# Performance work log

Measured on AMD Instinct MI355X. Metric: run time of the kernel, lower is better.

## Reference

```python
import math
import jax, jax.numpy as jnp
import numpy as np

NUM_HEADS = 16


def apply_rope(x, cos, sin):
    """x: (B,H,S,D); cos,sin: (S,D). Interleaved-pair rotation, matching torch code:
    uses even-indexed entries of cos/sin for both halves of each pair."""
    x1 = x[..., ::2]          # (B,H,S,D/2)
    x2 = x[..., 1::2]
    c = cos[:, ::2]           # (S,D/2)
    s = sin[:, ::2]
    rx_even = x1 * c - x2 * s
    rx_odd = x1 * s + x2 * c
    return jnp.stack([rx_even, rx_odd], axis=-1).reshape(x.shape)


def setup_inputs() -> dict:
    key = jax.random.key(0)
    ks = jax.random.split(key, 4)
    B, S, E = 4, 1024, 1024
    H, D = NUM_HEADS, E // NUM_HEADS
    x = jax.random.normal(ks[0], (B, S, E), dtype=jnp.float32)
    # realistic RoPE tables
    inv_freq = 1.0 / (10000.0 ** (np.arange(0, D, 2, dtype=np.float32) / D))
    pos = np.arange(S, dtype=np.float32)
    ang = pos[:, None] * inv_freq[None, :]            # (S, D/2)
    ang = np.repeat(ang, 2, axis=-1)                  # (S, D)
    cos = jnp.asarray(np.cos(ang), dtype=jnp.float32)
    sin = jnp.asarray(np.sin(ang), dtype=jnp.float32)
    attn_mask = jnp.zeros((S, S), dtype=jnp.float32)
    w_qkv = jax.random.normal(ks[1], (3 * E, E), dtype=jnp.float32) * (E ** -0.5)
    w_out = jax.random.normal(ks[2], (E, E), dtype=jnp.float32) * (E ** -0.5)
    b_out = jnp.zeros((E,), dtype=jnp.float32)
    return {"x": x, "attn_mask": attn_mask, "cos": cos, "sin": sin,
            "w_qkv": w_qkv, "w_out": w_out, "b_out": b_out}


def reference(x, attn_mask, cos, sin, w_qkv, w_out, b_out):
    B, S, E = x.shape
    H = NUM_HEADS
    D = E // H
    qkv = x @ w_qkv.T                                  # (B,S,3E)
    qkv = qkv.reshape(B, S, 3, H, D).transpose(2, 0, 3, 1, 4)  # (3,B,H,S,D)
    q, k, v = qkv[0], qkv[1], qkv[2]
    q = apply_rope(q, cos, sin)
    k = apply_rope(k, cos, sin)
    scores = jnp.einsum('bhqd,bhkd->bhqk', q, k) / math.sqrt(D)
    scores = scores + attn_mask                        # broadcast (S,S)
    attn = jax.nn.softmax(scores, axis=-1)
    out = jnp.einsum('bhqk,bhkd->bhqd', attn, v)
    out = out.transpose(0, 2, 1, 3).reshape(B, S, E)   # (B,S,E)
    return out @ w_out.T + b_out, attn
```

## Files before the change

kernel.cpp:

```cpp
#include <hip/hip_runtime.h>
#include <hip/hip_bf16.h>
#include <math.h>

#define S_ 1024
#define E_ 1024
#define H_ 16
#define D_ 64

typedef __attribute__((ext_vector_type(8))) short sv8;
typedef __attribute__((ext_vector_type(4))) short sv4;
typedef __attribute__((ext_vector_type(4))) float f4;

__device__ __forceinline__ short f2b(float f) {
  union { __hip_bfloat16 h; short s; } u;
  u.h = __float2bfloat16(f);
  return u.s;
}

__global__ void k_cvt(const float* __restrict__ x, const float* __restrict__ wqkv,
                      const float* __restrict__ wout, short* __restrict__ dst) {
  const long total = 8388608 / 4;
  for (long i = (long)blockIdx.x * blockDim.x + threadIdx.x; i < total;
       i += (long)gridDim.x * blockDim.x) {
    const long e = i * 4;
    float4 v;
    if (e < 4194304L)       v = *(const float4*)&x[e];
    else if (e < 7340032L)  v = *(const float4*)&wqkv[e - 4194304L];
    else                    v = *(const float4*)&wout[e - 7340032L];
    sv4 o;
    o[0] = f2b(v.x); o[1] = f2b(v.y); o[2] = f2b(v.z); o[3] = f2b(v.w);
    *(sv4*)&dst[e] = o;
  }
}

__global__ __launch_bounds__(256) void k_qkv_rope(
    const short* __restrict__ Xb, const short* __restrict__ Wb,
    const float* __restrict__ cosb, const float* __restrict__ sinb,
    short* __restrict__ qk, short* __restrict__ vT) {
  const int t = threadIdx.x;
  const int w = t >> 6, lane = t & 63, lr = lane & 15, lh = lane >> 4;
  const int m_w = blockIdx.y * 128 + (w & 1) * 64;
  const int n_w = blockIdx.x * 128 + (w >> 1) * 64;
  f4 acc[4][4] = {};
  for (int k0 = 0; k0 < 1024; k0 += 32) {
    sv8 a[4], b[4];
#pragma unroll
    for (int mt = 0; mt < 4; ++mt)
      a[mt] = *(const sv8*)&Xb[(size_t)(m_w + mt * 16 + lr) * 1024 + k0 + lh * 8];
#pragma unroll
    for (int nt = 0; nt < 4; ++nt)
      b[nt] = *(const sv8*)&Wb[(size_t)(n_w + nt * 16 + lr) * 1024 + k0 + lh * 8];
#pragma unroll
    for (int mt = 0; mt < 4; ++mt)
#pragma unroll
      for (int nt = 0; nt < 4; ++nt)
        acc[mt][nt] = __builtin_amdgcn_mfma_f32_16x16x32_bf16(a[mt], b[nt], acc[mt][nt], 0, 0, 0);
  }
#pragma unroll
  for (int nt = 0; nt < 4; ++nt) {
    const int n = n_w + nt * 16 + lr;
    const int which = n >> 10;
    const int e = n & 1023, h = e >> 6, d = e & 63;
#pragma unroll
    for (int mt = 0; mt < 4; ++mt) {
#pragma unroll
      for (int g = 0; g < 4; ++g) {
        const int m = m_w + mt * 16 + lh * 4 + g;
        const int bb = m >> 10, s = m & 1023;
        float v = acc[mt][nt][g];
        if (which < 2) {
          const float part = __shfl_xor(v, 1);
          const float c = cosb[s * 64 + (d & ~1)];
          const float sn = sinb[s * 64 + (d & ~1)];
          v = (d & 1) ? (part * sn + v * c) : (v * c - part * sn);
          qk[(size_t)which * 4194304 + ((size_t)((bb * 16 + h) * 1024 + s)) * 64 + d] = f2b(v);
        } else {
          vT[((size_t)((bb * 16 + h) * 64 + d)) * 1024 + s] = f2b(v);
        }
      }
    }
  }
}

__global__ __launch_bounds__(256) void k_attn(
    const short* __restrict__ qk, const short* __restrict__ vT,
    const float* __restrict__ mask, float* __restrict__ attn,
    short* __restrict__ ows) {
  __shared__ float Pl[4][32][68];
  __shared__ float redm[4][32], reds[4][32];
  const int t = threadIdx.x;
  const int w = t >> 6, lane = t & 63, lr = lane & 15, lh = lane >> 4;
  const int bh = blockIdx.y, q0 = blockIdx.x * 32;
  const int b = bh >> 4, h = bh & 15;
  const short* q = qk;
  const short* kk = qk + 4194304;

  sv8 qa[2][2];
#pragma unroll
  for (int mt = 0; mt < 2; ++mt)
#pragma unroll
    for (int kt = 0; kt < 2; ++kt)
      qa[mt][kt] = *(const sv8*)&q[((size_t)bh * 1024 + q0 + mt * 16 + lr) * 64 + kt * 32 + lh * 8];

  f4 acc[2][16] = {};
#pragma unroll
  for (int ct = 0; ct < 16; ++ct) {
    sv8 kb[2];
#pragma unroll
    for (int kt = 0; kt < 2; ++kt)
      kb[kt] = *(const sv8*)&kk[((size_t)bh * 1024 + w * 256 + ct * 16 + lr) * 64 + kt * 32 + lh * 8];
#pragma unroll
    for (int mt = 0; mt < 2; ++mt)
#pragma unroll
      for (int kt = 0; kt < 2; ++kt)
        acc[mt][ct] = __builtin_amdgcn_mfma_f32_16x16x32_bf16(qa[mt][kt], kb[kt], acc[mt][ct], 0, 0, 0);
  }

#pragma unroll
  for (int mt = 0; mt < 2; ++mt)
#pragma unroll
    for (int ct = 0; ct < 16; ++ct)
#pragma unroll
      for (int g = 0; g < 4; ++g)
        acc[mt][ct][g] = acc[mt][ct][g] * 0.125f +
            mask[(size_t)(q0 + mt * 16 + lh * 4 + g) * 1024 + w * 256 + ct * 16 + lr];

#pragma unroll
  for (int mt = 0; mt < 2; ++mt)
#pragma unroll
    for (int g = 0; g < 4; ++g) {
      float m = -1e30f;
#pragma unroll
      for (int ct = 0; ct < 16; ++ct) m = fmaxf(m, acc[mt][ct][g]);
      m = fmaxf(m, __shfl_xor(m, 1));
      m = fmaxf(m, __shfl_xor(m, 2));
      m = fmaxf(m, __shfl_xor(m, 4));
      m = fmaxf(m, __shfl_xor(m, 8));
      if (lr == 0) redm[w][mt * 16 + lh * 4 + g] = m;
    }
  __syncthreads();

#pragma unroll
  for (int mt = 0; mt < 2; ++mt)
#pragma unroll
    for (int g = 0; g < 4; ++g) {
      const int row = mt * 16 + lh * 4 + g;
      const float m = fmaxf(fmaxf(redm[0][row], redm[1][row]),
                            fmaxf(redm[2][row], redm[3][row]));
      float s = 0.f;
#pragma unroll
      for (int ct = 0; ct < 16; ++ct) {
        const float e = __expf(acc[mt][ct][g] - m);
        acc[mt][ct][g] = e;
        s += e;
      }
      s += __shfl_xor(s, 1);
      s += __shfl_xor(s, 2);
      s += __shfl_xor(s, 4);
      s += __shfl_xor(s, 8);
      if (lr == 0) reds[w][row] = s;
    }
  __syncthreads();

#pragma unroll
  for (int mt = 0; mt < 2; ++mt)
#pragma unroll
    for (int g = 0; g < 4; ++g) {
      const int row = mt * 16 + lh * 4 + g;
      const float r = 1.f / (reds[0][row] + reds[1][row] + reds[2][row] + reds[3][row]);
#pragma unroll
      for (int ct = 0; ct < 16; ++ct) {
        const float p = acc[mt][ct][g] * r;
        acc[mt][ct][g] = p;
        attn[((size_t)bh * 1024 + q0 + row) * 1024 + w * 256 + ct * 16 + lr] = p;
      }
    }

  f4 of[2][4] = {};
  for (int sc = 0; sc < 4; ++sc) {
    asm volatile("s_waitcnt lgkmcnt(0)" ::: "memory");
#pragma unroll
    for (int mt = 0; mt < 2; ++mt)
#pragma unroll
      for (int ci = 0; ci < 4; ++ci)
#pragma unroll
        for (int g = 0; g < 4; ++g)
          Pl[w][mt * 16 + lh * 4 + g][ci * 16 + lr] = acc[mt][sc * 4 + ci][g];
#pragma unroll
    for (int ktl = 0; ktl < 2; ++ktl) {
      sv8 pa[2];
#pragma unroll
      for (int mt = 0; mt < 2; ++mt) {
        const float* pp = &Pl[w][mt * 16 + lr][ktl * 32 + lh * 8];
        const float4 x0 = *(const float4*)pp;
        const float4 x1 = *(const float4*)(pp + 4);
        sv8 r;
        r[0] = f2b(x0.x); r[1] = f2b(x0.y); r[2] = f2b(x0.z); r[3] = f2b(x0.w);
        r[4] = f2b(x1.x); r[5] = f2b(x1.y); r[6] = f2b(x1.z); r[7] = f2b(x1.w);
        pa[mt] = r;
      }
#pragma unroll
      for (int nt = 0; nt < 4; ++nt) {
        const sv8 vb = *(const sv8*)&vT[((size_t)bh * 64 + nt * 16 + lr) * 1024 +
                                        w * 256 + sc * 64 + ktl * 32 + lh * 8];
#pragma unroll
        for (int mt = 0; mt < 2; ++mt)
          of[mt][nt] = __builtin_amdgcn_mfma_f32_16x16x32_bf16(pa[mt], vb, of[mt][nt], 0, 0, 0);
      }
    }
  }

  asm volatile("s_waitcnt lgkmcnt(0)" ::: "memory");
#pragma unroll
  for (int mt = 0; mt < 2; ++mt)
#pragma unroll
    for (int nt = 0; nt < 4; ++nt)
#pragma unroll
      for (int g = 0; g < 4; ++g)
        Pl[w][mt * 16 + lh * 4 + g][nt * 16 + lr] = of[mt][nt][g];
  __syncthreads();
  {
    const int row = t >> 3, c8 = (t & 7) * 8;
    sv8 oa;
#pragma unroll
    for (int j = 0; j < 8; ++j) {
      const float v = Pl[0][row][c8 + j] + Pl[1][row][c8 + j] +
                      Pl[2][row][c8 + j] + Pl[3][row][c8 + j];
      oa[j] = f2b(v);
    }
    *(sv8*)&ows[((size_t)(b * 1024) + q0 + row) * 1024 + h * 64 + c8] = oa;
  }
}

__global__ __launch_bounds__(256) void k_outproj(
    const short* __restrict__ Ob, const short* __restrict__ Wb,
    const float* __restrict__ bout, float* __restrict__ out) {
  const int t = threadIdx.x;
  const int w = t >> 6, lane = t & 63, lr = lane & 15, lh = lane >> 4;
  const int m_w = blockIdx.y * 128 + (w & 1) * 64;
  const int n_w = blockIdx.x * 128 + (w >> 1) * 64;
  f4 acc[4][4] = {};
  for (int k0 = 0; k0 < 1024; k0 += 32) {
    sv8 a[4], b[4];
#pragma unroll
    for (int mt = 0; mt < 4; ++mt)
      a[mt] = *(const sv8*)&Ob[(size_t)(m_w + mt * 16 + lr) * 1024 + k0 + lh * 8];
#pragma unroll
    for (int nt = 0; nt < 4; ++nt)
      b[nt] = *(const sv8*)&Wb[(size_t)(n_w + nt * 16 + lr) * 1024 + k0 + lh * 8];
#pragma unroll
    for (int mt = 0; mt < 4; ++mt)
#pragma unroll
      for (int nt = 0; nt < 4; ++nt)
        acc[mt][nt] = __builtin_amdgcn_mfma_f32_16x16x32_bf16(a[mt], b[nt], acc[mt][nt], 0, 0, 0);
  }
#pragma unroll
  for (int nt = 0; nt < 4; ++nt) {
    const int n = n_w + nt * 16 + lr;
    const float bb = bout[n];
#pragma unroll
    for (int mt = 0; mt < 4; ++mt)
#pragma unroll
      for (int g = 0; g < 4; ++g) {
        const int m = m_w + mt * 16 + lh * 4 + g;
        out[(size_t)m * 1024 + n] = acc[mt][nt][g] + bb;
      }
  }
}

extern "C" void kernel_launch(void* const* d_in, const int* in_sizes, int n_in,
                              void* d_out, int out_size, void* d_ws, size_t ws_size,
                              hipStream_t stream) {
  const float* x    = (const float*)d_in[0];
  const float* mask = (const float*)d_in[1];
  const float* cosb = (const float*)d_in[2];
  const float* sinb = (const float*)d_in[3];
  const float* wqkv = (const float*)d_in[4];
  const float* wout = (const float*)d_in[5];
  const float* bout = (const float*)d_in[6];

  float* out  = (float*)d_out;
  float* attn = out + (size_t)4194304;

  short* wsb   = (short*)d_ws;
  short* xb    = wsb;
  short* wqkvb = wsb + 4194304L;
  short* woutb = wsb + 7340032L;
  short* qk    = wsb + 8388608L;
  short* vT    = wsb + 16777216L;
  short* ows   = wsb + 20971520L;

  k_cvt<<<2048, 256, 0, stream>>>(x, wqkv, wout, xb);
  k_qkv_rope<<<dim3(24, 32), 256, 0, stream>>>(xb, wqkvb, cosb, sinb, qk, vT);
  k_attn<<<dim3(32, 64), 256, 0, stream>>>(qk, vT, mask, attn, ows);
  k_outproj<<<dim3(8, 32), 256, 0, stream>>>(ows, woutb, bout, out);
}
```

Before: 615.3 us.

## Stage GEMM tiles in LDS via direct loads and transpose attention score layout

Both GEMM kernels now load shared 128x32 A/B tiles into LDS with global_load_lds, so the four waves of a block share operands instead of each re-reading them from global memory. The attention kernel swaps MFMA operands so each lane holds four contiguous key columns, which allows float4 mask reads and float4 attn stores. It also writes P to LDS once as packed bf16 with an XOR swizzle, replacing the repeated fp32 staging and conversion. The cost is two block barriers per k-step with no double buffering, which exposes load latency.

After: 532.5 us. 13.5% less time.

```diff
diff --git a/kernel.cpp b/kernel.cpp
--- a/kernel.cpp
+++ b/kernel.cpp
@@ -2,19 +2,21 @@
 #include <hip/hip_bf16.h>
 #include <math.h>
 
-#define S_ 1024
-#define E_ 1024
-#define H_ 16
-#define D_ 64
-
 typedef __attribute__((ext_vector_type(8))) short sv8;
 typedef __attribute__((ext_vector_type(4))) short sv4;
 typedef __attribute__((ext_vector_type(4))) float f4;
+
+typedef __attribute__((address_space(3))) void lds_void_t;
+typedef __attribute__((address_space(1))) void g_void_t;
+#define GLD16(gp, lp) __builtin_amdgcn_global_load_lds((g_void_t*)(gp), (lds_void_t*)(lp), 16, 0, 0)
 
 __device__ __forceinline__ short f2b(float f) {
   union { __hip_bfloat16 h; short s; } u;
   u.h = __float2bfloat16(f);
   return u.s;
+}
+__device__ __forceinline__ unsigned pk2(float a, float b) {
+  return ((unsigned)(unsigned short)f2b(b) << 16) | (unsigned)(unsigned short)f2b(a);
 }
 
 __global__ void k_cvt(const float* __restrict__ x, const float* __restrict__ wqkv,
@@ -37,19 +39,28 @@
     const short* __restrict__ Xb, const short* __restrict__ Wb,
     const float* __restrict__ cosb, const float* __restrict__ sinb,
     short* __restrict__ qk, short* __restrict__ vT) {
+  __shared__ short As[4096], Bs[4096];
   const int t = threadIdx.x;
   const int w = t >> 6, lane = t & 63, lr = lane & 15, lh = lane >> 4;
-  const int m_w = blockIdx.y * 128 + (w & 1) * 64;
-  const int n_w = blockIdx.x * 128 + (w >> 1) * 64;
+  const int m0 = blockIdx.y * 128, n0 = blockIdx.x * 128;
+  const int mw = (w >> 1) * 64, nw = (w & 1) * 64;
   f4 acc[4][4] = {};
+  const int o0 = w * 1024 + lane * 16;
+  const int r0 = o0 >> 6, cb0 = o0 & 63;
+  const int o1 = o0 + 4096;
+  const int r1 = o1 >> 6, cb1 = o1 & 63;
   for (int k0 = 0; k0 < 1024; k0 += 32) {
+    __syncthreads();
+    GLD16((const char*)Xb + ((size_t)(m0 + r0) * 1024 + k0) * 2 + cb0, (char*)As + w * 1024);
+    GLD16((const char*)Wb + ((size_t)(n0 + r0) * 1024 + k0) * 2 + cb0, (char*)Bs + w * 1024);
+    GLD16((const char*)Xb + ((size_t)(m0 + r1) * 1024 + k0) * 2 + cb1, (char*)As + w * 1024 + 4096);
+    GLD16((const char*)Wb + ((size_t)(n0 + r1) * 1024 + k0) * 2 + cb1, (char*)Bs + w * 1024 + 4096);
+    __syncthreads();
     sv8 a[4], b[4];
 #pragma unroll
-    for (int mt = 0; mt < 4; ++mt)
-      a[mt] = *(const sv8*)&Xb[(size_t)(m_w + mt * 16 + lr) * 1024 + k0 + lh * 8];
-#pragma unroll
-    for (int nt = 0; nt < 4; ++nt)
-      b[nt] = *(const sv8*)&Wb[(size_t)(n_w + nt * 16 + lr) * 1024 + k0 + lh * 8];
+    for (int mt = 0; mt < 4; ++mt) a[mt] = *(const sv8*)&As[(mw + mt * 16 + lr) * 32 + lh * 8];
+#pragma unroll
+    for (int nt = 0; nt < 4; ++nt) b[nt] = *(const sv8*)&Bs[(nw + nt * 16 + lr) * 32 + lh * 8];
 #pragma unroll
     for (int mt = 0; mt < 4; ++mt)
 #pragma unroll
@@ -58,14 +69,14 @@
   }
 #pragma unroll
   for (int nt = 0; nt < 4; ++nt) {
-    const int n = n_w + nt * 16 + lr;
+    const int n = n0 + nw + nt * 16 + lr;
     const int which = n >> 10;
     const int e = n & 1023, h = e >> 6, d = e & 63;
 #pragma unroll
-    for (int mt = 0; mt < 4; ++mt) {
+    for (int mt = 0; mt < 4; ++mt)
 #pragma unroll
       for (int g = 0; g < 4; ++g) {
-        const int m = m_w + mt * 16 + lh * 4 + g;
+        const int m = m0 + mw + mt * 16 + lh * 4 + g;
         const int bb = m >> 10, s = m & 1023;
         float v = acc[mt][nt][g];
         if (which < 2) {
@@ -78,7 +89,6 @@
           vT[((size_t)((bb * 16 + h) * 64 + d)) * 1024 + s] = f2b(v);
         }
       }
-    }
   }
 }
 
@@ -86,7 +96,7 @@
     const short* __restrict__ qk, const short* __restrict__ vT,
     const float* __restrict__ mask, float* __restrict__ attn,
     short* __restrict__ ows) {
-  __shared__ float Pl[4][32][68];
+  __shared__ short Pbs[4 * 32 * 256];
   __shared__ float redm[4][32], reds[4][32];
   const int t = threadIdx.x;
   const int w = t >> 6, lane = t & 63, lr = lane & 15, lh = lane >> 4;
@@ -97,10 +107,10 @@
 
   sv8 qa[2][2];
 #pragma unroll
-  for (int mt = 0; mt < 2; ++mt)
+  for (int qt = 0; qt < 2; ++qt)
 #pragma unroll
     for (int kt = 0; kt < 2; ++kt)
-      qa[mt][kt] = *(const sv8*)&q[((size_t)bh * 1024 + q0 + mt * 16 + lr) * 64 + kt * 32 + lh * 8];
+      qa[qt][kt] = *(const sv8*)&q[((size_t)bh * 1024 + q0 + qt * 16 + lr) * 64 + kt * 32 + lh * 8];
 
   f4 acc[2][16] = {};
 #pragma unroll
@@ -110,122 +120,107 @@
     for (int kt = 0; kt < 2; ++kt)
       kb[kt] = *(const sv8*)&kk[((size_t)bh * 1024 + w * 256 + ct * 16 + lr) * 64 + kt * 32 + lh * 8];
 #pragma unroll
-    for (int mt = 0; mt < 2; ++mt)
+    for (int qt = 0; qt < 2; ++qt)
 #pragma unroll
       for (int kt = 0; kt < 2; ++kt)
-        acc[mt][ct] = __builtin_amdgcn_mfma_f32_16x16x32_bf16(qa[mt][kt], kb[kt], acc[mt][ct], 0, 0, 0);
-  }
-
-#pragma unroll
-  for (int mt = 0; mt < 2; ++mt)
+        acc[qt][ct] = __builtin_amdgcn_mfma_f32_16x16x32_bf16(kb[kt], qa[qt][kt], acc[qt][ct], 0, 0, 0);
+  }
+
+#pragma unroll
+  for (int qt = 0; qt < 2; ++qt)
+#pragma unroll
+    for (int ct = 0; ct < 16; ++ct) {
+      const float4 mv = *(const float4*)&mask[(size_t)(q0 + qt * 16 + lr) * 1024 + w * 256 + ct * 16 + lh * 4];
+      acc[qt][ct][0] = acc[qt][ct][0] * 0.125f + mv.x;
+      acc[qt][ct][1] = acc[qt][ct][1] * 0.125f + mv.y;
+      acc[qt][ct][2] = acc[qt][ct][2] * 0.125f + mv.z;
+      acc[qt][ct][3] = acc[qt][ct][3] * 0.125f + mv.w;
+    }
+
+#pragma unroll
+  for (int qt = 0; qt < 2; ++qt) {
+    float m = -1e30f;
 #pragma unroll
     for (int ct = 0; ct < 16; ++ct)
 #pragma unroll
-      for (int g = 0; g < 4; ++g)
-        acc[mt][ct][g] = acc[mt][ct][g] * 0.125f +
-            mask[(size_t)(q0 + mt * 16 + lh * 4 + g) * 1024 + w * 256 + ct * 16 + lr];
-
-#pragma unroll
-  for (int mt = 0; mt < 2; ++mt)
-#pragma unroll
-    for (int g = 0; g < 4; ++g) {
-      float m = -1e30f;
-#pragma unroll
-      for (int ct = 0; ct < 16; ++ct) m = fmaxf(m, acc[mt][ct][g]);
-      m = fmaxf(m, __shfl_xor(m, 1));
-      m = fmaxf(m, __shfl_xor(m, 2));
-      m = fmaxf(m, __shfl_xor(m, 4));
-      m = fmaxf(m, __shfl_xor(m, 8));
-      if (lr == 0) redm[w][mt * 16 + lh * 4 + g] = m;
-    }
+      for (int g = 0; g < 4; ++g) m = fmaxf(m, acc[qt][ct][g]);
+    m = fmaxf(m, __shfl_xor(m, 16));
+    m = fmaxf(m, __shfl_xor(m, 32));
+    if (lane < 16) redm[w][qt * 16 + lr] = m;
+  }
   __syncthreads();
 
 #pragma unroll
-  for (int mt = 0; mt < 2; ++mt)
-#pragma unroll
-    for (int g = 0; g < 4; ++g) {
-      const int row = mt * 16 + lh * 4 + g;
-      const float m = fmaxf(fmaxf(redm[0][row], redm[1][row]),
-                            fmaxf(redm[2][row], redm[3][row]));
-      float s = 0.f;
-#pragma unroll
-      for (int ct = 0; ct < 16; ++ct) {
-        const float e = __expf(acc[mt][ct][g] - m);
-        acc[mt][ct][g] = e;
+  for (int qt = 0; qt < 2; ++qt) {
+    const int row = qt * 16 + lr;
+    const float gm = fmaxf(fmaxf(redm[0][row], redm[1][row]),
+                           fmaxf(redm[2][row], redm[3][row]));
+    float s = 0.f;
+#pragma unroll
+    for (int ct = 0; ct < 16; ++ct)
+#pragma unroll
+      for (int g = 0; g < 4; ++g) {
+        const float e = __expf(acc[qt][ct][g] - gm);
+        acc[qt][ct][g] = e;
         s += e;
       }
-      s += __shfl_xor(s, 1);
-      s += __shfl_xor(s, 2);
-      s += __shfl_xor(s, 4);
-      s += __shfl_xor(s, 8);
-      if (lr == 0) reds[w][row] = s;
-    }
+    s += __shfl_xor(s, 16);
+    s += __shfl_xor(s, 32);
+    if (lane < 16) reds[w][row] = s;
+  }
   __syncthreads();
 
 #pragma unroll
-  for (int mt = 0; mt < 2; ++mt)
-#pragma unroll
-    for (int g = 0; g < 4; ++g) {
-      const int row = mt * 16 + lh * 4 + g;
-      const float r = 1.f / (reds[0][row] + reds[1][row] + reds[2][row] + reds[3][row]);
-#pragma unroll
-      for (int ct = 0; ct < 16; ++ct) {
-        const float p = acc[mt][ct][g] * r;
-        acc[mt][ct][g] = p;
-        attn[((size_t)bh * 1024 + q0 + row) * 1024 + w * 256 + ct * 16 + lr] = p;
-      }
-    }
+  for (int qt = 0; qt < 2; ++qt) {
+    const int row = qt * 16 + lr;
+    const float r = 1.f / (reds[0][row] + reds[1][row] + reds[2][row] + reds[3][row]);
+#pragma unroll
+    for (int ct = 0; ct < 16; ++ct) {
+      const float p0 = acc[qt][ct][0] * r, p1 = acc[qt][ct][1] * r;
+      const float p2 = acc[qt][ct][2] * r, p3 = acc[qt][ct][3] * r;
+      float4 st; st.x = p0; st.y = p1; st.z = p2; st.w = p3;
+      *(float4*)&attn[((size_t)bh * 1024 + q0 + row) * 1024 + w * 256 + ct * 16 + lh * 4] = st;
+      const int col = ct * 16 + lh * 4;
+      uint2 u; u.x = pk2(p0, p1); u.y = pk2(p2, p3);
+      *(uint2*)&Pbs[(w * 32 + row) * 256 + (col ^ ((row & 7) << 3))] = u;
+    }
+  }
 
   f4 of[2][4] = {};
-  for (int sc = 0; sc < 4; ++sc) {
-    asm volatile("s_waitcnt lgkmcnt(0)" ::: "memory");
-#pragma unroll
-    for (int mt = 0; mt < 2; ++mt)
-#pragma unroll
-      for (int ci = 0; ci < 4; ++ci)
-#pragma unroll
-        for (int g = 0; g < 4; ++g)
-          Pl[w][mt * 16 + lh * 4 + g][ci * 16 + lr] = acc[mt][sc * 4 + ci][g];
-#pragma unroll
-    for (int ktl = 0; ktl < 2; ++ktl) {
-      sv8 pa[2];
-#pragma unroll
-      for (int mt = 0; mt < 2; ++mt) {
-        const float* pp = &Pl[w][mt * 16 + lr][ktl * 32 + lh * 8];
-        const float4 x0 = *(const float4*)pp;
-        const float4 x1 = *(const float4*)(pp + 4);
-        sv8 r;
-        r[0] = f2b(x0.x); r[1] = f2b(x0.y); r[2] = f2b(x0.z); r[3] = f2b(x0.w);
-        r[4] = f2b(x1.x); r[5] = f2b(x1.y); r[6] = f2b(x1.z); r[7] = f2b(x1.w);
-        pa[mt] = r;
-      }
-#pragma unroll
-      for (int nt = 0; nt < 4; ++nt) {
-        const sv8 vb = *(const sv8*)&vT[((size_t)bh * 64 + nt * 16 + lr) * 1024 +
-                                        w * 256 + sc * 64 + ktl * 32 + lh * 8];
-#pragma unroll
-        for (int mt = 0; mt < 2; ++mt)
-          of[mt][nt] = __builtin_amdgcn_mfma_f32_16x16x32_bf16(pa[mt], vb, of[mt][nt], 0, 0, 0);
-      }
-    }
-  }
-
-  asm volatile("s_waitcnt lgkmcnt(0)" ::: "memory");
-#pragma unroll
-  for (int mt = 0; mt < 2; ++mt)
+  for (int ks = 0; ks < 8; ++ks) {
+    sv8 pa[2];
+#pragma unroll
+    for (int qt = 0; qt < 2; ++qt) {
+      const int row = qt * 16 + lr;
+      const int col = ks * 32 + lh * 8;
+      pa[qt] = *(const sv8*)&Pbs[(w * 32 + row) * 256 + (col ^ ((row & 7) << 3))];
+    }
+#pragma unroll
+    for (int nt = 0; nt < 4; ++nt) {
+      const sv8 vb = *(const sv8*)&vT[((size_t)bh * 64 + nt * 16 + lr) * 1024 + w * 256 + ks * 32 + lh * 8];
+#pragma unroll
+      for (int qt = 0; qt < 2; ++qt)
+        of[qt][nt] = __builtin_amdgcn_mfma_f32_16x16x32_bf16(pa[qt], vb, of[qt][nt], 0, 0, 0);
+    }
+  }
+
+  __syncthreads();
+  float* Ol = (float*)Pbs;
+#pragma unroll
+  for (int qt = 0; qt < 2; ++qt)
 #pragma unroll
     for (int nt = 0; nt < 4; ++nt)
 #pragma unroll
       for (int g = 0; g < 4; ++g)
-        Pl[w][mt * 16 + lh * 4 + g][nt * 16 + lr] = of[mt][nt][g];
+        Ol[(w * 32 + qt * 16 + lh * 4 + g) * 68 + nt * 16 + lr] = of[qt][nt][g];
   __syncthreads();
   {
     const int row = t >> 3, c8 = (t & 7) * 8;
     sv8 oa;
 #pragma unroll
     for (int j = 0; j < 8; ++j) {
-      const float v = Pl[0][row][c8 + j] + Pl[1][row][c8 + j] +
-                      Pl[2][row][c8 + j] + Pl[3][row][c8 + j];
+      const float v = Ol[(0 * 32 + row) * 68 + c8 + j] + Ol[(1 * 32 + row) * 68 + c8 + j] +
+                      Ol[(2 * 32 + row) * 68 + c8 + j] + Ol[(3 * 32 + row) * 68 + c8 + j];
       oa[j] = f2b(v);
     }
     *(sv8*)&ows[((size_t)(b * 1024) + q0 + row) * 1024 + h * 64 + c8] = oa;
@@ -235,19 +230,28 @@
 __global__ __launch_bounds__(256) void k_outproj(
     const short* __restrict__ Ob, const short* __restrict__ Wb,
     const float* __restrict__ bout, float* __restrict__ out) {
+  __shared__ short As[4096], Bs[4096];
   const int t = threadIdx.x;
   const int w = t >> 6, lane = t & 63, lr = lane & 15, lh = lane >> 4;
-  const int m_w = blockIdx.y * 128 + (w & 1) * 64;
-  const int n_w = blockIdx.x * 128 + (w >> 1) * 64;
+  const int m0 = blockIdx.y * 128, n0 = blockIdx.x * 128;
+  const int mw = (w >> 1) * 64, nw = (w & 1) * 64;
   f4 acc[4][4] = {};
+  const int o0 = w * 1024 + lane * 16;
+  const int r0 = o0 >> 6, cb0 = o0 & 63;
+  const int o1 = o0 + 4096;
+  const int r1 = o1 >> 6, cb1 = o1 & 63;
   for (int k0 = 0; k0 < 1024; k0 += 32) {
+    __syncthreads();
+    GLD16((const char*)Ob + ((size_t)(m0 + r0) * 1024 + k0) * 2 + cb0, (char*)As + w * 1024);
+    GLD16((const char*)Wb + ((size_t)(n0 + r0) * 1024 + k0) * 2 + cb0, (char*)Bs + w * 1024);
+    GLD16((const char*)Ob + ((size_t)(m0 + r1) * 1024 + k0) * 2 + cb1, (char*)As + w * 1024 + 4096);
+    GLD16((const char*)Wb + ((size_t)(n0 + r1) * 1024 + k0) * 2 + cb1, (char*)Bs + w * 1024 + 4096);
+    __syncthreads();
     sv8 a[4], b[4];
 #pragma unroll
-    for (int mt = 0; mt < 4; ++mt)
-      a[mt] = *(const sv8*)&Ob[(size_t)(m_w + mt * 16 + lr) * 1024 + k0 + lh * 8];
-#pragma unroll
-    for (int nt = 0; nt < 4; ++nt)
-      b[nt] = *(const sv8*)&Wb[(size_t)(n_w + nt * 16 + lr) * 1024 + k0 + lh * 8];
+    for (int mt = 0; mt < 4; ++mt) a[mt] = *(const sv8*)&As[(mw + mt * 16 + lr) * 32 + lh * 8];
+#pragma unroll
+    for (int nt = 0; nt < 4; ++nt) b[nt] = *(const sv8*)&Bs[(nw + nt * 16 + lr) * 32 + lh * 8];
 #pragma unroll
     for (int mt = 0; mt < 4; ++mt)
 #pragma unroll
@@ -256,13 +260,13 @@
   }
 #pragma unroll
   for (int nt = 0; nt < 4; ++nt) {
-    const int n = n_w + nt * 16 + lr;
+    const int n = n0 + nw + nt * 16 + lr;
     const float bb = bout[n];
 #pragma unroll
     for (int mt = 0; mt < 4; ++mt)
 #pragma unroll
       for (int g = 0; g < 4; ++g) {
-        const int m = m_w + mt * 16 + lh * 4 + g;
+        const int m = m0 + mw + mt * 16 + lh * 4 + g;
         out[(size_t)m * 1024 + n] = acc[mt][nt][g] + bb;
       }
   }
```
